# Kernel tuning notes

Measured on AMD Instinct MI355X. Metric: run time of the kernel, lower is better.

Reference implementation:

```python
import jax, jax.numpy as jnp
import numpy as np
import math

N_NODES = 50000
N_EDGES = 1600000
DIM = 64
HEADS = 8
EDGE_DIM = 32


def setup_inputs() -> dict:
    key = jax.random.key(0)
    ks = jax.random.split(key, 12)
    s = 1.0 / math.sqrt(DIM)
    se = 1.0 / math.sqrt(EDGE_DIM)
    return {
        'x': jax.random.normal(ks[0], (N_NODES, DIM), jnp.float32),
        'edge_index': jax.random.randint(ks[1], (2, N_EDGES), 0, N_NODES),
        'edge_attr': jax.random.normal(ks[2], (N_EDGES, EDGE_DIM), jnp.float32),
        'WQ': jax.random.normal(ks[3], (DIM, DIM), jnp.float32) * s,
        'bQ': jnp.zeros((DIM,), jnp.float32),
        'WK': jax.random.normal(ks[4], (DIM, DIM), jnp.float32) * s,
        'bK': jnp.zeros((DIM,), jnp.float32),
        'WV': jax.random.normal(ks[5], (DIM, DIM), jnp.float32) * s,
        'bV': jnp.zeros((DIM,), jnp.float32),
        'WO': jax.random.normal(ks[6], (DIM, DIM), jnp.float32) * s,
        'bO': jnp.zeros((DIM,), jnp.float32),
        'We1': jax.random.normal(ks[7], (EDGE_DIM, EDGE_DIM), jnp.float32) * se,
        'be1': jnp.zeros((EDGE_DIM,), jnp.float32),
        'We2': jax.random.normal(ks[8], (EDGE_DIM, HEADS), jnp.float32) * se,
        'be2': jnp.zeros((HEADS,), jnp.float32),
    }


def graph_softmax(src, index, num_segments):
    # src: [E, H], index: [E] -> per-destination-node stable softmax
    smax = jax.ops.segment_max(src, index, num_segments=num_segments)  # [N, H]
    smax = jnp.where(jnp.isfinite(smax), smax, 0.0)  # nodes with no edges
    e = jnp.exp(src - smax[index])
    ssum = jax.ops.segment_sum(e, index, num_segments=num_segments) + 1e-12
    return e / ssum[index]


def reference(x, edge_index, edge_attr, WQ, bQ, WK, bK, WV, bV, WO, bO, We1, be1, We2, be2):
    num_nodes = x.shape[0]
    d_k = DIM // HEADS
    i, j = edge_index[0], edge_index[1]
    # per-node projections [N, H, d_k], then gather per-edge
    Q = (x @ WQ + bQ).reshape(num_nodes, HEADS, d_k)
    K = (x @ WK + bK).reshape(num_nodes, HEADS, d_k)
    V = (x @ WV + bV).reshape(num_nodes, HEADS, d_k)
    query = Q[j]  # [E, H, d_k]
    key = K[i]
    value = V[i]
    # edge bias MLP: [edge_dim -> edge_dim -> num_heads] with SiLU between
    h = jax.nn.silu(edge_attr @ We1 + be1)
    bias = h @ We2 + be2  # [E, H]
    scores = jnp.sum(query * key, axis=-1) / math.sqrt(d_k) + bias  # [E, H]
    alpha = graph_softmax(scores, j, num_nodes)  # [E, H]
    weighted = (alpha[..., None] * value).reshape(-1, DIM)  # [E, dim]
    attn_out = jax.ops.segment_sum(weighted, j, num_segments=num_nodes)  # [N, dim]
    return attn_out @ WO + bO
```

## Files before the change

### kernel.cpp

```cpp
#include <hip/hip_runtime.h>
#include <math.h>

#define N_NODES 50000
#define N_EDGES 1600000
#define DIM 64
#define HEADS 8
#define EDGE_DIM 32

#define NB 256
#define NPB 196
#define ACAP 8192
#define PART_T 256
#define EPT 8
#define PART_E (PART_T * EPT)

#define QKV_BLKS 12500

typedef __fp16 h2 __attribute__((ext_vector_type(2)));

__device__ __forceinline__ unsigned int f2bf(float f) {
    union { float f; unsigned int u; } c; c.f = f;
    unsigned int u = c.u;
    return (u + 0x7FFFu + ((u >> 16) & 1u)) >> 16;
}
__device__ __forceinline__ float bf_lo(unsigned int u) { return __uint_as_float(u << 16); }
__device__ __forceinline__ float bf_hi(unsigned int u) { return __uint_as_float(u & 0xFFFF0000u); }
__device__ __forceinline__ unsigned int h2u(h2 v) { union { h2 h; unsigned int u; } c; c.h = v; return c.u; }
__device__ __forceinline__ h2 u2h(unsigned int x) { union { h2 h; unsigned int u; } c; c.u = x; return c.h; }

__global__ __launch_bounds__(1024) void pack_weights(
    const float* __restrict__ We1, const float* __restrict__ We2,
    h2* __restrict__ w1p, h2* __restrict__ w2p, int* __restrict__ gcur)
{
    const int t = threadIdx.x;
    if (t < 512) {
        const int c = t >> 4, kk = t & 15;
        w1p[t] = __builtin_amdgcn_cvt_pkrtz(We1[(2 * kk) * EDGE_DIM + c],
                                            We1[(2 * kk + 1) * EDGE_DIM + c]);
    } else if (t < 512 + 128) {
        const int u = t - 512;
        const int h = u >> 4, cc = u & 15;
        w2p[u] = __builtin_amdgcn_cvt_pkrtz(We2[(2 * cc) * HEADS + h],
                                            We2[(2 * cc + 1) * HEADS + h]);
    } else if (t >= 768 && t < 768 + NB) {
        gcur[t - 768] = 0;
    }
}

__global__ __launch_bounds__(256) void mlp_only(
    const float* __restrict__ edge_attr,
    const h2* __restrict__ w1p, const float* __restrict__ be1,
    const h2* __restrict__ w2p, const float* __restrict__ be2,
    uint4* __restrict__ bias_by_e)
{
    const int e = blockIdx.x * 256 + threadIdx.x;
    if (e >= N_EDGES) return;
    float a[EDGE_DIM];
    const float4* ar = (const float4*)(edge_attr + (size_t)e * EDGE_DIM);
    #pragma unroll
    for (int q = 0; q < EDGE_DIM / 4; ++q) {
        float4 v = ar[q];
        a[q * 4 + 0] = v.x; a[q * 4 + 1] = v.y;
        a[q * 4 + 2] = v.z; a[q * 4 + 3] = v.w;
    }
    h2 a2[EDGE_DIM / 2];
    #pragma unroll
    for (int kk = 0; kk < EDGE_DIM / 2; ++kk)
        a2[kk] = __builtin_amdgcn_cvt_pkrtz(a[2 * kk], a[2 * kk + 1]);
    float sil[EDGE_DIM];
    #pragma unroll 8
    for (int c = 0; c < EDGE_DIM; ++c) {
        float s = be1[c];
        #pragma unroll
        for (int kk = 0; kk < EDGE_DIM / 2; ++kk)
            s = __builtin_amdgcn_fdot2(a2[kk], w1p[c * 16 + kk], s, false);
        sil[c] = __fdividef(s, 1.0f + __expf(-s));
    }
    h2 s2[EDGE_DIM / 2];
    #pragma unroll
    for (int cc = 0; cc < EDGE_DIM / 2; ++cc)
        s2[cc] = __builtin_amdgcn_cvt_pkrtz(sil[2 * cc], sil[2 * cc + 1]);
    float b0f = be2[0], b1f = be2[1], b2f = be2[2], b3f = be2[3];
    float b4f = be2[4], b5f = be2[5], b6f = be2[6], b7f = be2[7];
    #pragma unroll
    for (int cc = 0; cc < EDGE_DIM / 2; ++cc) {
        b0f = __builtin_amdgcn_fdot2(s2[cc], w2p[0 * 16 + cc], b0f, false);
        b1f = __builtin_amdgcn_fdot2(s2[cc], w2p[1 * 16 + cc], b1f, false);
        b2f = __builtin_amdgcn_fdot2(s2[cc], w2p[2 * 16 + cc], b2f, false);
        b3f = __builtin_amdgcn_fdot2(s2[cc], w2p[3 * 16 + cc], b3f, false);
        b4f = __builtin_amdgcn_fdot2(s2[cc], w2p[4 * 16 + cc], b4f, false);
        b5f = __builtin_amdgcn_fdot2(s2[cc], w2p[5 * 16 + cc], b5f, false);
        b6f = __builtin_amdgcn_fdot2(s2[cc], w2p[6 * 16 + cc], b6f, false);
        b7f = __builtin_amdgcn_fdot2(s2[cc], w2p[7 * 16 + cc], b7f, false);
    }
    uint4 br;
    br.x = f2bf(b0f) | (f2bf(b1f) << 16);
    br.y = f2bf(b2f) | (f2bf(b3f) << 16);
    br.z = f2bf(b4f) | (f2bf(b5f) << 16);
    br.w = f2bf(b6f) | (f2bf(b7f) << 16);
    bias_by_e[e] = br;
}

__global__ __launch_bounds__(256) void partition_only(
    const int* __restrict__ ei, int* __restrict__ gcur, uint2* __restrict__ A_rec)
{
    __shared__ int cnt[NB];
    __shared__ int base[NB];
    __shared__ int lbase[NB];
    __shared__ int wsum[4];
    __shared__ int total_s;
    __shared__ uint2 srec[PART_E];
    __shared__ unsigned char sbkt[PART_E];
    const int tid = threadIdx.x;
    const int lane = tid & 63;
    const int w = tid >> 6;
    cnt[tid] = 0;
    __syncthreads();
    const int e0 = blockIdx.x * PART_E;
    #pragma unroll
    for (int k = 0; k < EPT; ++k) {
        const int e = e0 + k * PART_T + tid;
        if (e < N_EDGES) atomicAdd(&cnt[ei[N_EDGES + e] / NPB], 1);
    }
    __syncthreads();
    int v = cnt[tid];
    #pragma unroll
    for (int o = 1; o < 64; o <<= 1) {
        int t = __shfl_up(v, o, 64);
        if (lane >= o) v += t;
    }
    if (lane == 63) wsum[w] = v;
    __syncthreads();
    int add = 0;
    #pragma unroll
    for (int ww = 0; ww < 3; ++ww) if (ww < w) add += wsum[ww];
    v += add;
    {
        const int c = cnt[tid];
        base[tid] = (c > 0) ? atomicAdd(&gcur[tid], c) : 0;
        lbase[tid] = v - c;
        if (tid == NB - 1) total_s = v;
        cnt[tid] = 0;
    }
    __syncthreads();
    #pragma unroll
    for (int k = 0; k < EPT; ++k) {
        const int e = e0 + k * PART_T + tid;
        if (e < N_EDGES) {
            const int i = ei[e];
            const int j = ei[N_EDGES + e];
            const int b = j / NPB;
            const int jl = j - b * NPB;
            const int s = lbase[b] + atomicAdd(&cnt[b], 1);
            srec[s] = make_uint2((unsigned)e, ((unsigned)jl << 24) | (unsigned)i);
            sbkt[s] = (unsigned char)b;
        }
    }
    __syncthreads();
    const int total = total_s;
    for (int s = tid; s < total; s += PART_T) {
        const int b = sbkt[s];
        const int gp = base[b] + (s - lbase[b]);
        if (gp < ACAP) A_rec[(size_t)b * ACAP + gp] = srec[s];
    }
}

__global__ __launch_bounds__(256) void perm_qkv(
    const int* __restrict__ gcur, const uint2* __restrict__ A_rec,
    const uint4* __restrict__ bias_by_e,
    int* __restrict__ offs, int* __restrict__ src_sorted,
    uint4* __restrict__ bias_sorted,
    const float* __restrict__ x,
    const float* __restrict__ WQ, const float* __restrict__ bQ,
    const float* __restrict__ WK, const float* __restrict__ bK,
    const float* __restrict__ WV, const float* __restrict__ bV,
    unsigned int* __restrict__ Q2, unsigned int* __restrict__ KV2)
{
    __shared__ __align__(16) char smem[3 * DIM * DIM * sizeof(float)];
    const int tid = threadIdx.x;
    const int lane = tid & 63;
    const int w = tid >> 6;
    if (blockIdx.x < NB) {
        int* ldeg = (int*)smem;
        int* loff = ldeg + NPB;
        int* wsum = loff + NPB + 1;
        int* gb   = wsum + 4;
        const int b = blockIdx.x;
        if (w == 0) {
            int ssum = 0;
            for (int t = lane; t < b; t += 64) ssum += min(gcur[t], ACAP);
            #pragma unroll
            for (int o = 1; o < 64; o <<= 1) ssum += __shfl_xor(ssum, o, 64);
            if (lane == 0) gb[0] = ssum;
        }
        if (tid < NPB) ldeg[tid] = 0;
        __syncthreads();
        const int gbase = gb[0];
        const int nb = min(gcur[b], ACAP);
        for (int r = tid; r < nb; r += 256)
            atomicAdd(&ldeg[A_rec[(size_t)b * ACAP + r].y >> 24], 1);
        __syncthreads();
        int v = (tid < NPB) ? ldeg[tid] : 0;
        #pragma unroll
        for (int o = 1; o < 64; o <<= 1) {
            int t = __shfl_up(v, o, 64);
            if (lane >= o) v += t;
        }
        if (lane == 63) wsum[w] = v;
        __syncthreads();
        int add = 0;
        #pragma unroll
        for (int ww = 0; ww < 3; ++ww) if (ww < w) add += wsum[ww];
        v += add;
        if (tid == 0) loff[0] = 0;
        if (tid < NPB) { loff[tid + 1] = v; ldeg[tid] = 0; }
        __syncthreads();
        const int jbase = b * NPB;
        if (tid < NPB && jbase + tid < N_NODES) offs[jbase + tid] = gbase + loff[tid];
        if (b == NB - 1 && tid == 0) offs[N_NODES] = gbase + nb;
        for (int r = tid; r < nb; r += 256) {
            const uint2 rec = A_rec[(size_t)b * ACAP + r];
            const int jl = (int)(rec.y >> 24);
            const int slot = loff[jl] + atomicAdd(&ldeg[jl], 1);
            const int gp = gbase + slot;
            src_sorted[gp] = (int)(rec.y & 0xFFFFFFu);
            bias_sorted[gp] = bias_by_e[rec.x];
        }
    } else {
        float* sWQ = (float*)smem;
        float* sWK = sWQ + DIM * DIM;
        float* sWV = sWK + DIM * DIM;
        for (int t = tid; t < DIM * DIM; t += 256) {
            sWQ[t] = WQ[t]; sWK[t] = WK[t]; sWV[t] = WV[t];
        }
        __syncthreads();
        const int n = (blockIdx.x - NB) * 4 + w;
        if (n >= N_NODES) return;
        float xl = x[(size_t)n * DIM + lane];
        float aq = bQ[lane], ak = bK[lane], av = bV[lane];
        #pragma unroll
        for (int k = 0; k < DIM; ++k) {
            float xv = __shfl(xl, k, 64);
            aq += xv * sWQ[k * DIM + lane];
            ak += xv * sWK[k * DIM + lane];
            av += xv * sWV[k * DIM + lane];
        }
        const int s = lane & 31;
        const float aq_e = __shfl(aq, 2 * s, 64);
        const float aq_o = __shfl(aq, 2 * s + 1, 64);
        const float ak_e = __shfl(ak, 2 * s, 64);
        const float ak_o = __shfl(ak, 2 * s + 1, 64);
        const float av_e = __shfl(av, 2 * s, 64);
        const float av_o = __shfl(av, 2 * s + 1, 64);
        if (lane < 32) {
            Q2[(size_t)n * 32 + s]  = h2u(__builtin_amdgcn_cvt_pkrtz(aq_e, aq_o));
            KV2[(size_t)n * 64 + s] = h2u(__builtin_amdgcn_cvt_pkrtz(ak_e, ak_o));
        } else {
            KV2[(size_t)n * 64 + 32 + s] = f2bf(av_e) | (f2bf(av_o) << 16);
        }
    }
}

__global__ __launch_bounds__(256) void node_attn_out(
    const int* __restrict__ off,
    const int* __restrict__ src_sorted,
    const unsigned short* __restrict__ bias_u16,
    const unsigned int* __restrict__ Q2, const unsigned int* __restrict__ KV2,
    const float* __restrict__ WO, const float* __restrict__ bO,
    float* __restrict__ out)
{
    __shared__ float sWO[DIM * DIM];
    for (int t = threadIdx.x; t < DIM * DIM; t += 256) sWO[t] = WO[t];
    __syncthreads();
    const int lane = threadIdx.x & 63;
    const int wave = threadIdx.x >> 6;
    const int j = blockIdx.x * 4 + wave;
    if (j >= N_NODES) return;
    const int beg = off[j], end = off[j + 1];
    const int s = lane & 31;
    const int half = lane >> 5;
    const int h = s >> 2;
    const float inv_sqrt_dk = 0.35355339059327373f;
    const h2 q2 = u2h(Q2[(size_t)j * 32 + s]);
    float num2x = 0.0f, num2y = 0.0f;
    float den = 1e-12f;
    int t = beg;
    for (; t + 7 < end; t += 8) {
        int iv[4];
        unsigned int k2v[4], v2v[4];
        float bb[4], d[4];
        #pragma unroll
        for (int q = 0; q < 4; ++q) iv[q] = src_sorted[t + 2 * q + half];
        #pragma unroll
        for (int q = 0; q < 4; ++q) k2v[q] = KV2[(size_t)iv[q] * 64 + s];
        #pragma unroll
        for (int q = 0; q < 4; ++q) v2v[q] = KV2[(size_t)iv[q] * 64 + 32 + s];
        #pragma unroll
        for (int q = 0; q < 4; ++q)
            bb[q] = bf_lo((unsigned int)bias_u16[(size_t)(t + 2 * q + half) * HEADS + h]);
        #pragma unroll
        for (int q = 0; q < 4; ++q)
            d[q] = __builtin_amdgcn_fdot2(q2, u2h(k2v[q]), 0.0f, false);
        #pragma unroll
        for (int q = 0; q < 4; ++q) d[q] += __shfl_xor(d[q], 1, 64);
        #pragma unroll
        for (int q = 0; q < 4; ++q) d[q] += __shfl_xor(d[q], 2, 64);
        #pragma unroll
        for (int q = 0; q < 4; ++q) {
            const float ev = __expf(d[q] * inv_sqrt_dk + bb[q]);
            num2x += ev * bf_lo(v2v[q]);
            num2y += ev * bf_hi(v2v[q]);
            den += ev;
        }
    }
    for (; t + 1 < end; t += 2) {
        const int iv = src_sorted[t + half];
        const unsigned int k2v = KV2[(size_t)iv * 64 + s];
        const unsigned int v2v = KV2[(size_t)iv * 64 + 32 + s];
        const float bb = bf_lo((unsigned int)bias_u16[(size_t)(t + half) * HEADS + h]);
        float d = __builtin_amdgcn_fdot2(q2, u2h(k2v), 0.0f, false);
        d += __shfl_xor(d, 1, 64);
        d += __shfl_xor(d, 2, 64);
        const float ev = __expf(d * inv_sqrt_dk + bb);
        num2x += ev * bf_lo(v2v);
        num2y += ev * bf_hi(v2v);
        den += ev;
    }
    if (t < end) {
        const int iv = src_sorted[t];
        const unsigned int k2v = KV2[(size_t)iv * 64 + s];
        const unsigned int v2v = KV2[(size_t)iv * 64 + 32 + s];
        const float bb = bf_lo((unsigned int)bias_u16[(size_t)t * HEADS + h]);
        float d = __builtin_amdgcn_fdot2(q2, u2h(k2v), 0.0f, false);
        d += __shfl_xor(d, 1, 64);
        d += __shfl_xor(d, 2, 64);
        float ev = __expf(d * inv_sqrt_dk + bb);
        if (half != 0) ev = 0.0f;
        num2x += ev * bf_lo(v2v);
        num2y += ev * bf_hi(v2v);
        den += ev;
    }
    num2x += __shfl_xor(num2x, 32, 64);
    num2y += __shfl_xor(num2y, 32, 64);
    den   += __shfl_xor(den, 32, 64);
    const float av2x = num2x / den;
    const float av2y = num2y / den;
    float acc = bO[lane];
    #pragma unroll
    for (int sp = 0; sp < 32; ++sp) {
        acc += __shfl(av2x, sp, 64) * sWO[(2 * sp) * DIM + lane];
        acc += __shfl(av2y, sp, 64) * sWO[(2 * sp + 1) * DIM + lane];
    }
    out[(size_t)j * DIM + lane] = acc;
}

extern "C" void kernel_launch(void* const* d_in, const int* in_sizes, int n_in,
                              void* d_out, int out_size, void* d_ws, size_t ws_size,
                              hipStream_t stream) {
    const float* x    = (const float*)d_in[0];
    const int*   ei   = (const int*)d_in[1];
    const float* ea   = (const float*)d_in[2];
    const float* WQ   = (const float*)d_in[3];
    const float* bQ   = (const float*)d_in[4];
    const float* WK   = (const float*)d_in[5];
    const float* bK   = (const float*)d_in[6];
    const float* WV   = (const float*)d_in[7];
    const float* bV   = (const float*)d_in[8];
    const float* WO   = (const float*)d_in[9];
    const float* bO   = (const float*)d_in[10];
    const float* We1  = (const float*)d_in[11];
    const float* be1  = (const float*)d_in[12];
    const float* We2  = (const float*)d_in[13];
    const float* be2  = (const float*)d_in[14];
    float* out = (float*)d_out;

    char* ws = (char*)d_ws;
    size_t off_b = 0;
    auto alloc = [&](size_t bytes) {
        void* p = ws + off_b;
        off_b += (bytes + 255) & ~(size_t)255;
        return p;
    };
    unsigned int* Q2          = (unsigned int*)alloc((size_t)N_NODES * 32 * sizeof(unsigned int));
    unsigned int* KV2         = (unsigned int*)alloc((size_t)N_NODES * 64 * sizeof(unsigned int));
    uint2*        A_rec       = (uint2*)alloc((size_t)NB * ACAP * sizeof(uint2));
    uint4*        bias_by_e   = (uint4*)alloc((size_t)N_EDGES * sizeof(uint4));
    uint4*        bias_sorted = (uint4*)alloc((size_t)N_EDGES * sizeof(uint4));
    int*          src_sorted  = (int*)alloc((size_t)N_EDGES * sizeof(int));
    int*          offs        = (int*)alloc((size_t)(N_NODES + 1) * sizeof(int));
    int*          gcur        = (int*)alloc((size_t)NB * sizeof(int));
    h2*           w1p         = (h2*)alloc(512 * sizeof(h2));
    h2*           w2p         = (h2*)alloc(128 * sizeof(h2));

    pack_weights<<<1, 1024, 0, stream>>>(We1, We2, w1p, w2p, gcur);
    partition_only<<<(N_EDGES + PART_E - 1) / PART_E, PART_T, 0, stream>>>(ei, gcur, A_rec);
    mlp_only<<<(N_EDGES + 255) / 256, 256, 0, stream>>>(ea, w1p, be1, w2p, be2, bias_by_e);
    perm_qkv<<<NB + QKV_BLKS, 256, 0, stream>>>(gcur, A_rec, bias_by_e,
                                                offs, src_sorted, bias_sorted,
                                                x, WQ, bQ, WK, bK, WV, bV, Q2, KV2);
    node_attn_out<<<(N_NODES + 3) / 4, 256, 0, stream>>>(offs, src_sorted,
                                                         (const unsigned short*)bias_sorted,
                                                         Q2, KV2, WO, bO, out);
}
```

Before: 303.4 us.

## Drop the bias permutation and gather bias by original edge id in attention

The permutation kernel no longer copies each edge's 16-byte bias into destination-sorted order. It now writes a packed (edge id, source) record per edge, and the attention kernel reads the bias straight from the unsorted per-edge buffer using the edge id. This removes one large sorted-bias array and its scattered write, at the cost of random bias reads inside the attention loop. Separately, the partition is made finer: twice as many buckets with half as many nodes each, smaller capacity per bucket, and 512-thread partition blocks.

Measured after the change: 291.1 us. 1.04x faster.

```diff
diff --git a/kernel.cpp b/kernel.cpp
--- a/kernel.cpp
+++ b/kernel.cpp
@@ -7,11 +7,11 @@
 #define HEADS 8
 #define EDGE_DIM 32
 
-#define NB 256
-#define NPB 196
-#define ACAP 8192
-#define PART_T 256
-#define EPT 8
+#define NB 512
+#define NPB 98
+#define ACAP 4096
+#define PART_T 512
+#define EPT 4
 #define PART_E (PART_T * EPT)
 
 #define QKV_BLKS 12500
@@ -42,9 +42,8 @@
         const int h = u >> 4, cc = u & 15;
         w2p[u] = __builtin_amdgcn_cvt_pkrtz(We2[(2 * cc) * HEADS + h],
                                             We2[(2 * cc + 1) * HEADS + h]);
-    } else if (t >= 768 && t < 768 + NB) {
-        gcur[t - 768] = 0;
-    }
+    }
+    if (t < NB) gcur[t] = 0;
 }
 
 __global__ __launch_bounds__(256) void mlp_only(
@@ -101,16 +100,16 @@
     bias_by_e[e] = br;
 }
 
-__global__ __launch_bounds__(256) void partition_only(
+__global__ __launch_bounds__(512) void partition_only(
     const int* __restrict__ ei, int* __restrict__ gcur, uint2* __restrict__ A_rec)
 {
     __shared__ int cnt[NB];
     __shared__ int base[NB];
     __shared__ int lbase[NB];
-    __shared__ int wsum[4];
+    __shared__ int wsum[8];
     __shared__ int total_s;
     __shared__ uint2 srec[PART_E];
-    __shared__ unsigned char sbkt[PART_E];
+    __shared__ unsigned short sbkt[PART_E];
     const int tid = threadIdx.x;
     const int lane = tid & 63;
     const int w = tid >> 6;
@@ -133,7 +132,7 @@
     __syncthreads();
     int add = 0;
     #pragma unroll
-    for (int ww = 0; ww < 3; ++ww) if (ww < w) add += wsum[ww];
+    for (int ww = 0; ww < 7; ++ww) if (ww < w) add += wsum[ww];
     v += add;
     {
         const int c = cnt[tid];
@@ -153,7 +152,7 @@
             const int jl = j - b * NPB;
             const int s = lbase[b] + atomicAdd(&cnt[b], 1);
             srec[s] = make_uint2((unsigned)e, ((unsigned)jl << 24) | (unsigned)i);
-            sbkt[s] = (unsigned char)b;
+            sbkt[s] = (unsigned short)b;
         }
     }
     __syncthreads();
@@ -167,9 +166,7 @@
 
 __global__ __launch_bounds__(256) void perm_qkv(
     const int* __restrict__ gcur, const uint2* __restrict__ A_rec,
-    const uint4* __restrict__ bias_by_e,
-    int* __restrict__ offs, int* __restrict__ src_sorted,
-    uint4* __restrict__ bias_sorted,
+    int* __restrict__ offs, uint2* __restrict__ es_sorted,
     const float* __restrict__ x,
     const float* __restrict__ WQ, const float* __restrict__ bQ,
     const float* __restrict__ WK, const float* __restrict__ bK,
@@ -222,9 +219,7 @@
             const uint2 rec = A_rec[(size_t)b * ACAP + r];
             const int jl = (int)(rec.y >> 24);
             const int slot = loff[jl] + atomicAdd(&ldeg[jl], 1);
-            const int gp = gbase + slot;
-            src_sorted[gp] = (int)(rec.y & 0xFFFFFFu);
-            bias_sorted[gp] = bias_by_e[rec.x];
+            es_sorted[(size_t)gbase + slot] = make_uint2(rec.x, rec.y & 0xFFFFFFu);
         }
     } else {
         float* sWQ = (float*)smem;
@@ -263,7 +258,7 @@
 
 __global__ __launch_bounds__(256) void node_attn_out(
     const int* __restrict__ off,
-    const int* __restrict__ src_sorted,
+    const uint2* __restrict__ es_sorted,
     const unsigned short* __restrict__ bias_u16,
     const unsigned int* __restrict__ Q2, const unsigned int* __restrict__ KV2,
     const float* __restrict__ WO, const float* __restrict__ bO,
@@ -286,18 +281,18 @@
     float den = 1e-12f;
     int t = beg;
     for (; t + 7 < end; t += 8) {
-        int iv[4];
+        uint2 r[4];
         unsigned int k2v[4], v2v[4];
         float bb[4], d[4];
         #pragma unroll
-        for (int q = 0; q < 4; ++q) iv[q] = src_sorted[t + 2 * q + half];
-        #pragma unroll
-        for (int q = 0; q < 4; ++q) k2v[q] = KV2[(size_t)iv[q] * 64 + s];
-        #pragma unroll
-        for (int q = 0; q < 4; ++q) v2v[q] = KV2[(size_t)iv[q] * 64 + 32 + s];
+        for (int q = 0; q < 4; ++q) r[q] = es_sorted[t + 2 * q + half];
+        #pragma unroll
+        for (int q = 0; q < 4; ++q) k2v[q] = KV2[(size_t)r[q].y * 64 + s];
+        #pragma unroll
+        for (int q = 0; q < 4; ++q) v2v[q] = KV2[(size_t)r[q].y * 64 + 32 + s];
         #pragma unroll
         for (int q = 0; q < 4; ++q)
-            bb[q] = bf_lo((unsigned int)bias_u16[(size_t)(t + 2 * q + half) * HEADS + h]);
+            bb[q] = bf_lo((unsigned int)bias_u16[(size_t)r[q].x * HEADS + h]);
         #pragma unroll
         for (int q = 0; q < 4; ++q)
             d[q] = __builtin_amdgcn_fdot2(q2, u2h(k2v[q]), 0.0f, false);
@@ -314,10 +309,10 @@
         }
     }
     for (; t + 1 < end; t += 2) {
-        const int iv = src_sorted[t + half];
-        const unsigned int k2v = KV2[(size_t)iv * 64 + s];
-        const unsigned int v2v = KV2[(size_t)iv * 64 + 32 + s];
-        const float bb = bf_lo((unsigned int)bias_u16[(size_t)(t + half) * HEADS + h]);
+        const uint2 r0 = es_sorted[t + half];
+        const unsigned int k2v = KV2[(size_t)r0.y * 64 + s];
+        const unsigned int v2v = KV2[(size_t)r0.y * 64 + 32 + s];
+        const float bb = bf_lo((unsigned int)bias_u16[(size_t)r0.x * HEADS + h]);
         float d = __builtin_amdgcn_fdot2(q2, u2h(k2v), 0.0f, false);
         d += __shfl_xor(d, 1, 64);
         d += __shfl_xor(d, 2, 64);
@@ -327,10 +322,10 @@
         den += ev;
     }
     if (t < end) {
-        const int iv = src_sorted[t];
-        const unsigned int k2v = KV2[(size_t)iv * 64 + s];
-        const unsigned int v2v = KV2[(size_t)iv * 64 + 32 + s];
-        const float bb = bf_lo((unsigned int)bias_u16[(size_t)t * HEADS + h]);
+        const uint2 r0 = es_sorted[t];
+        const unsigned int k2v = KV2[(size_t)r0.y * 64 + s];
+        const unsigned int v2v = KV2[(size_t)r0.y * 64 + 32 + s];
+        const float bb = bf_lo((unsigned int)bias_u16[(size_t)r0.x * HEADS + h]);
         float d = __builtin_amdgcn_fdot2(q2, u2h(k2v), 0.0f, false);
         d += __shfl_xor(d, 1, 64);
         d += __shfl_xor(d, 2, 64);
@@ -381,24 +376,22 @@
         off_b += (bytes + 255) & ~(size_t)255;
         return p;
     };
-    unsigned int* Q2          = (unsigned int*)alloc((size_t)N_NODES * 32 * sizeof(unsigned int));
-    unsigned int* KV2         = (unsigned int*)alloc((size_t)N_NODES * 64 * sizeof(unsigned int));
-    uint2*        A_rec       = (uint2*)alloc((size_t)NB * ACAP * sizeof(uint2));
-    uint4*        bias_by_e   = (uint4*)alloc((size_t)N_EDGES * sizeof(uint4));
-    uint4*        bias_sorted = (uint4*)alloc((size_t)N_EDGES * sizeof(uint4));
-    int*          src_sorted  = (int*)alloc((size_t)N_EDGES * sizeof(int));
-    int*          offs        = (int*)alloc((size_t)(N_NODES + 1) * sizeof(int));
-    int*          gcur        = (int*)alloc((size_t)NB * sizeof(int));
-    h2*           w1p         = (h2*)alloc(512 * sizeof(h2));
-    h2*           w2p         = (h2*)alloc(128 * sizeof(h2));
+    unsigned int* Q2        = (unsigned int*)alloc((size_t)N_NODES * 32 * sizeof(unsigned int));
+    unsigned int* KV2       = (unsigned int*)alloc((size_t)N_NODES * 64 * sizeof(unsigned int));
+    uint2*        A_rec     = (uint2*)alloc((size_t)NB * ACAP * sizeof(uint2));
+    uint4*        bias_by_e = (uint4*)alloc((size_t)N_EDGES * sizeof(uint4));
+    uint2*        es_sorted = (uint2*)alloc((size_t)N_EDGES * sizeof(uint2));
+    int*          offs      = (int*)alloc((size_t)(N_NODES + 1) * sizeof(int));
+    int*          gcur      = (int*)alloc((size_t)NB * sizeof(int));
+    h2*           w1p       = (h2*)alloc(512 * sizeof(h2));
+    h2*           w2p       = (h2*)alloc(128 * sizeof(h2));
 
     pack_weights<<<1, 1024, 0, stream>>>(We1, We2, w1p, w2p, gcur);
     partition_only<<<(N_EDGES + PART_E - 1) / PART_E, PART_T, 0, stream>>>(ei, gcur, A_rec);
     mlp_only<<<(N_EDGES + 255) / 256, 256, 0, stream>>>(ea, w1p, be1, w2p, be2, bias_by_e);
-    perm_qkv<<<NB + QKV_BLKS, 256, 0, stream>>>(gcur, A_rec, bias_by_e,
-                                                offs, src_sorted, bias_sorted,
+    perm_qkv<<<NB + QKV_BLKS, 256, 0, stream>>>(gcur, A_rec, offs, es_sorted,
                                                 x, WQ, bQ, WK, bK, WV, bV, Q2, KV2);
-    node_attn_out<<<(N_NODES + 3) / 4, 256, 0, stream>>>(offs, src_sorted,
-                                                         (const unsigned short*)bias_sorted,
+    node_attn_out<<<(N_NODES + 3) / 4, 256, 0, stream>>>(offs, es_sorted,
+                                                         (const unsigned short*)bias_by_e,
                                                          Q2, KV2, WO, bO, out);
 }
```
